# Performance work log

Hardware: AMD Instinct MI355X
Metric: run time of the kernel (lower is better)

Reference implementation:

```python
import jax, jax.numpy as jnp
import numpy as np

N = 50000
E = 800000
IN_DIM = 256
HID = 64
HEADS = 4
OUT_DIM = 32
NEG_SLOPE = 0.2


def gat_conv(x, edge_index, W, a_src, a_dst, bias, heads, out_ch, concat):
    """PyG-style GATConv (eval mode, add_self_loops=True).
    x: [N, F_in]; edge_index: [2, E'] with row0=src, row1=dst.
    W: [F_in, heads*out_ch]; a_src/a_dst: [heads, out_ch]; bias: [heads*out_ch] or [out_ch].
    """
    n = x.shape[0]
    # add self loops
    loops = jnp.arange(n, dtype=edge_index.dtype)
    src = jnp.concatenate([edge_index[0], loops])
    dst = jnp.concatenate([edge_index[1], loops])

    h = (x @ W).reshape(n, heads, out_ch)              # [N, H, C]
    alpha_s = jnp.einsum('nhc,hc->nh', h, a_src)       # [N, H]
    alpha_d = jnp.einsum('nhc,hc->nh', h, a_dst)       # [N, H]
    e = alpha_s[src] + alpha_d[dst]                    # [E', H]
    e = jnp.where(e >= 0, e, NEG_SLOPE * e)            # leaky_relu

    # segment softmax over incoming edges of each dst node
    m = jax.ops.segment_max(e, dst, num_segments=n)    # [N, H]
    ex = jnp.exp(e - m[dst])
    denom = jax.ops.segment_sum(ex, dst, num_segments=n)
    alpha = ex / (denom[dst] + 1e-16)                  # [E', H]

    msg = h[src] * alpha[:, :, None]                   # [E', H, C]
    out = jax.ops.segment_sum(msg, dst, num_segments=n)  # [N, H, C]
    out = out.reshape(n, heads * out_ch) if concat else out.mean(axis=1)
    return out + bias


def setup_inputs() -> dict:
    key = jax.random.key(0)
    ks = jax.random.split(key, 10)
    x = jax.random.normal(ks[0], (N, IN_DIM), dtype=jnp.float32)
    edge_index = jax.random.randint(ks[1], (2, E), 0, N, dtype=jnp.int32)
    s1 = 1.0 / np.sqrt(IN_DIM)
    s2 = 1.0 / np.sqrt(HEADS * HID)
    return {
        'x': x,
        'edge_index': edge_index,
        'W1': jax.random.normal(ks[2], (IN_DIM, HEADS * HID), dtype=jnp.float32) * s1,
        'a_src1': jax.random.normal(ks[3], (HEADS, HID), dtype=jnp.float32) * s2,
        'a_dst1': jax.random.normal(ks[4], (HEADS, HID), dtype=jnp.float32) * s2,
        'b1': jnp.zeros((HEADS * HID,), dtype=jnp.float32),
        'W2': jax.random.normal(ks[5], (HEADS * HID, OUT_DIM), dtype=jnp.float32) * s2,
        'a_src2': jax.random.normal(ks[6], (1, OUT_DIM), dtype=jnp.float32) * 0.125,
        'a_dst2': jax.random.normal(ks[7], (1, OUT_DIM), dtype=jnp.float32) * 0.125,
        'b2': jnp.zeros((OUT_DIM,), dtype=jnp.float32),
    }


def reference(x, edge_index, W1, a_src1, a_dst1, b1, W2, a_src2, a_dst2, b2):
    h = gat_conv(x, edge_index, W1, a_src1, a_dst1, b1, HEADS, HID, concat=True)
    h = jax.nn.elu(h)
    out = gat_conv(h, edge_index, W2, a_src2, a_dst2, b2, 1, OUT_DIM, concat=False)
    return out
```

## Files before the change

kernel.cpp:

```cpp
#include <hip/hip_runtime.h>

#define NEG_SLOPE 0.2f
#define CAP 64
#define LOG2E 1.44269504f

typedef short bf16x8 __attribute__((ext_vector_type(8)));
typedef float f32x4 __attribute__((ext_vector_type(4)));
typedef _Float16 half4v __attribute__((ext_vector_type(4)));
typedef _Float16 half8v __attribute__((ext_vector_type(8)));

__device__ inline short bf16_rne(float x) {
    unsigned u = __float_as_uint(x);
    unsigned r = u + 0x7FFFu + ((u >> 16) & 1u);
    return (short)(r >> 16);
}

__device__ inline float fast_exp2(float x) {
#if __has_builtin(__builtin_amdgcn_exp2f)
    return __builtin_amdgcn_exp2f(x);
#else
    return exp2f(x);
#endif
}


__global__ void k_prepw(const float* __restrict__ W1, short* __restrict__ Wt,
                        const float* __restrict__ W2, _Float16* __restrict__ W2t,
                        int* __restrict__ cursor, int* __restrict__ col, int N) {
    int r = blockIdx.x;
    int t = threadIdx.x;
    Wt[(size_t)t * 256 + r] = bf16_rne(W1[(size_t)r * 256 + t]);
    if (t < 32) W2t[(size_t)t * 256 + r] = (_Float16)W2[(size_t)r * 32 + t];
    int gid = blockIdx.x * 256 + threadIdx.x;
    if (gid < N) {
        cursor[gid] = 1;
        col[(size_t)gid * CAP] = gid;
    }
}


__global__ __launch_bounds__(256) void k_gemm1_scatter(
        const float* __restrict__ x, const short* __restrict__ Wt,
        const float* __restrict__ a_src, const float* __restrict__ a_dst,
        _Float16* __restrict__ h1, float* __restrict__ as1, float* __restrict__ ad1, int N,
        const int* __restrict__ srcI, const int* __restrict__ dstI,
        int* __restrict__ cursor, int* __restrict__ col, int E) {
    __shared__ short Ab[64 * 40];
    __shared__ short Bb[256 * 40];
    const int tid = threadIdx.x;
    const int b = blockIdx.x;
    const int nGemm = gridDim.x;

    const int chunk = (E + nGemm - 1) / nGemm;
    const int ss = b * chunk;
    const int se = (ss + chunk < E) ? (ss + chunk) : E;
    const int jb = ss + tid * 4;
    int4 d4 = make_int4(0, 0, 0, 0), s4 = make_int4(0, 0, 0, 0);
    int p0 = CAP, p1 = CAP, p2 = CAP, p3 = CAP;
    const bool quad = (jb + 3 < se);
    if (quad) {
        d4 = *(const int4*)(dstI + jb);
        s4 = *(const int4*)(srcI + jb);
    } else if (jb < se) {
        for (int i = jb; i < se; ++i) {
            int d = dstI[i];
            int p = atomicAdd(&cursor[d], 1);
            if (p < CAP) col[(size_t)d * CAP + p] = srcI[i];
        }
    }

    const int lane = tid & 63;
    const int wc = tid >> 6;
    const int row0 = b * 64;
    const int m15 = lane & 15, quad4 = lane >> 4;

    f32x4 acc[4][4] = {};

    const int arow = tid >> 2;
    const int akseg = (tid & 3) * 8;

#pragma unroll
    for (int kk = 0; kk < 8; ++kk) {
        const int k0 = kk * 32;
        {
            int row = row0 + arow;
            float vals[8];
            if (row < N) {
                float4 v0 = *(const float4*)(x + (size_t)row * 256 + k0 + akseg);
                float4 v1 = *(const float4*)(x + (size_t)row * 256 + k0 + akseg + 4);
                vals[0] = v0.x; vals[1] = v0.y; vals[2] = v0.z; vals[3] = v0.w;
                vals[4] = v1.x; vals[5] = v1.y; vals[6] = v1.z; vals[7] = v1.w;
            } else {
#pragma unroll
                for (int i = 0; i < 8; ++i) vals[i] = 0.f;
            }
            short buf[8];
#pragma unroll
            for (int i = 0; i < 8; ++i) buf[i] = bf16_rne(vals[i]);
            *(bf16x8*)&Ab[arow * 40 + akseg] = *(bf16x8*)&buf[0];
        }
        {
#pragma unroll
            for (int s = 0; s < 4; ++s)
                *(bf16x8*)&Bb[tid * 40 + s * 8] =
                    *(const bf16x8*)(Wt + (size_t)tid * 256 + k0 + s * 8);
        }
        if (quad) {
            const int e = kk >> 1;
            const int d = (e == 0) ? d4.x : (e == 1) ? d4.y : (e == 2) ? d4.z : d4.w;
            if ((kk & 1) == 0) {
                int pr = atomicAdd(&cursor[d], 1);
                if (e == 0) p0 = pr; else if (e == 1) p1 = pr;
                else if (e == 2) p2 = pr; else p3 = pr;
            } else {
                const int s = (e == 0) ? s4.x : (e == 1) ? s4.y : (e == 2) ? s4.z : s4.w;
                const int pr = (e == 0) ? p0 : (e == 1) ? p1 : (e == 2) ? p2 : p3;
                if (pr < CAP) col[(size_t)d * CAP + pr] = s;
            }
        }
        __syncthreads();
        bf16x8 ab[4];
#pragma unroll
        for (int mt = 0; mt < 4; ++mt)
            ab[mt] = *(const bf16x8*)&Ab[(mt * 16 + m15) * 40 + quad4 * 8];
#pragma unroll
        for (int nt = 0; nt < 4; ++nt) {
            int nn = wc * 64 + nt * 16 + m15;
            bf16x8 bb = *(const bf16x8*)&Bb[nn * 40 + quad4 * 8];
#pragma unroll
            for (int mt = 0; mt < 4; ++mt)
                acc[mt][nt] = __builtin_amdgcn_mfma_f32_16x16x32_bf16(ab[mt], bb, acc[mt][nt], 0, 0, 0);
        }
        __syncthreads();
    }
    const int head = wc;
#pragma unroll
    for (int mt = 0; mt < 4; ++mt) {
        float va[4] = {0.f, 0.f, 0.f, 0.f};
        float vd[4] = {0.f, 0.f, 0.f, 0.f};
#pragma unroll
        for (int nt = 0; nt < 4; ++nt) {
            int colg = wc * 64 + nt * 16 + m15;
            float asv = a_src[colg];
            float adv = a_dst[colg];
#pragma unroll
            for (int r = 0; r < 4; ++r) {
                float accv = acc[mt][nt][r];
                int row = row0 + mt * 16 + quad4 * 4 + r;
                if (row < N) h1[(size_t)row * 256 + colg] = (_Float16)accv;
                va[r] = fmaf(accv, asv, va[r]);
                vd[r] = fmaf(accv, adv, vd[r]);
            }
        }
#pragma unroll
        for (int r = 0; r < 4; ++r) {
#pragma unroll
            for (int mq = 1; mq < 16; mq <<= 1) {
                va[r] += __shfl_xor(va[r], mq);
                vd[r] += __shfl_xor(vd[r], mq);
            }
            int row = row0 + mt * 16 + quad4 * 4 + r;
            if (m15 == 0 && row < N) {
                as1[(size_t)row * 4 + head] = va[r] * LOG2E;
                ad1[(size_t)row * 4 + head] = vd[r] * LOG2E;
            }
        }
    }
}


__global__ __launch_bounds__(256) void k_fuse1(
        const _Float16* __restrict__ h1, const float* __restrict__ as1,
        const float* __restrict__ ad1, const int* __restrict__ cursor,
        const int* __restrict__ col, const float* __restrict__ b1,
        const _Float16* __restrict__ W2t, const float* __restrict__ a_s2,
        const float* __restrict__ a_d2, _Float16* __restrict__ z,
        float* __restrict__ as2, float* __restrict__ ad2, int N) {
    __shared__ _Float16 W2s[32 * 264];
    __shared__ _Float16 h2s[4 * 256];
    const int tid = threadIdx.x;
    const int l = tid & 63;
    const int wave = tid >> 6;
    const int n = blockIdx.x * 4 + wave;

    for (int i8 = tid; i8 < 1024; i8 += 256) {
        int elem = i8 * 8;
        int row = elem >> 8, k = elem & 255;
        *(half8v*)&W2s[row * 264 + k] = *(const half8v*)(W2t + (size_t)row * 256 + k);
    }
    __syncthreads();
    if (n >= N) return;

    const int head = l >> 4;
    const int beg = n * CAP;
    int deg = __builtin_amdgcn_readfirstlane(cursor[n]);
    if (deg > CAP) deg = CAP;
    int colv = 0;
    if (l < deg) colv = col[beg + l];
    float adv = ad1[(size_t)n * 4 + head];

    f32x4 a0 = {}, a1 = {}, a2 = {}, a3 = {};
    float s0 = 0.f, s1 = 0.f, s2 = 0.f, s3 = 0.f;
    int j = 0;
    for (; j + 3 < deg; j += 4) {
        int c0 = __builtin_amdgcn_readlane(colv, j);
        int c1 = __builtin_amdgcn_readlane(colv, j + 1);
        int c2 = __builtin_amdgcn_readlane(colv, j + 2);
        int c3 = __builtin_amdgcn_readlane(colv, j + 3);
        float e0 = as1[(size_t)c0 * 4 + head] + adv;
        float e1 = as1[(size_t)c1 * 4 + head] + adv;
        float e2 = as1[(size_t)c2 * 4 + head] + adv;
        float e3 = as1[(size_t)c3 * 4 + head] + adv;
        e0 = fmaxf(e0, NEG_SLOPE * e0); e1 = fmaxf(e1, NEG_SLOPE * e1);
        e2 = fmaxf(e2, NEG_SLOPE * e2); e3 = fmaxf(e3, NEG_SLOPE * e3);
        float p0 = fast_exp2(e0), p1 = fast_exp2(e1);
        float p2 = fast_exp2(e2), p3 = fast_exp2(e3);
        half4v h0 = *((const half4v*)(h1 + (size_t)c0 * 256) + l);
        half4v hv1 = *((const half4v*)(h1 + (size_t)c1 * 256) + l);
        half4v h2 = *((const half4v*)(h1 + (size_t)c2 * 256) + l);
        half4v h3 = *((const half4v*)(h1 + (size_t)c3 * 256) + l);
        s0 += p0; s1 += p1; s2 += p2; s3 += p3;
        a0 += __builtin_convertvector(h0, f32x4) * p0;
        a1 += __builtin_convertvector(hv1, f32x4) * p1;
        a2 += __builtin_convertvector(h2, f32x4) * p2;
        a3 += __builtin_convertvector(h3, f32x4) * p3;
    }
    for (; j < deg; ++j) {
        int c0 = __builtin_amdgcn_readlane(colv, j);
        float e0 = as1[(size_t)c0 * 4 + head] + adv;
        e0 = fmaxf(e0, NEG_SLOPE * e0);
        float p0 = fast_exp2(e0);
        half4v h0 = *((const half4v*)(h1 + (size_t)c0 * 256) + l);
        s0 += p0;
        a0 += __builtin_convertvector(h0, f32x4) * p0;
    }
    f32x4 at = (a0 + a1) + (a2 + a3);
    float iv = 1.f / ((s0 + s1) + (s2 + s3) + 1e-16f);
    float4 bb = *(const float4*)(b1 + l * 4);
    float4 v;
    v.x = at[0] * iv + bb.x;
    v.y = at[1] * iv + bb.y;
    v.z = at[2] * iv + bb.z;
    v.w = at[3] * iv + bb.w;
    v.x = (v.x > 0.f) ? v.x : (__expf(v.x) - 1.f);
    v.y = (v.y > 0.f) ? v.y : (__expf(v.y) - 1.f);
    v.z = (v.z > 0.f) ? v.z : (__expf(v.z) - 1.f);
    v.w = (v.w > 0.f) ? v.w : (__expf(v.w) - 1.f);
    half4v hv;
    hv.x = (_Float16)v.x; hv.y = (_Float16)v.y; hv.z = (_Float16)v.z; hv.w = (_Float16)v.w;
    *((half4v*)(h2s + wave * 256) + l) = hv;

    int c = l & 31;
    int kh = (l >> 5) * 128;
    const _Float16* hrow = h2s + wave * 256 + kh;
    const _Float16* wrow = W2s + c * 264 + kh;
    float accz = 0.f;
#pragma unroll
    for (int k = 0; k < 128; k += 8) {
        half8v hz = *(const half8v*)(hrow + k);
        half8v wz = *(const half8v*)(wrow + k);
#if __has_builtin(__builtin_amdgcn_fdot2)
        accz = __builtin_amdgcn_fdot2(__builtin_shufflevector(hz, hz, 0, 1),
                                      __builtin_shufflevector(wz, wz, 0, 1), accz, false);
        accz = __builtin_amdgcn_fdot2(__builtin_shufflevector(hz, hz, 2, 3),
                                      __builtin_shufflevector(wz, wz, 2, 3), accz, false);
        accz = __builtin_amdgcn_fdot2(__builtin_shufflevector(hz, hz, 4, 5),
                                      __builtin_shufflevector(wz, wz, 4, 5), accz, false);
        accz = __builtin_amdgcn_fdot2(__builtin_shufflevector(hz, hz, 6, 7),
                                      __builtin_shufflevector(wz, wz, 6, 7), accz, false);
#else
        accz = fmaf((float)hz[0], (float)wz[0], accz);
        accz = fmaf((float)hz[1], (float)wz[1], accz);
        accz = fmaf((float)hz[2], (float)wz[2], accz);
        accz = fmaf((float)hz[3], (float)wz[3], accz);
        accz = fmaf((float)hz[4], (float)wz[4], accz);
        accz = fmaf((float)hz[5], (float)wz[5], accz);
        accz = fmaf((float)hz[6], (float)wz[6], accz);
        accz = fmaf((float)hz[7], (float)wz[7], accz);
#endif
    }
    accz += __shfl_xor(accz, 32);
    float za = accz * a_s2[c];
    float zd = accz * a_d2[c];
#pragma unroll
    for (int mq = 1; mq < 32; mq <<= 1) {
        za += __shfl_xor(za, mq);
        zd += __shfl_xor(zd, mq);
    }
    if (l < 32) z[(size_t)n * 32 + c] = (_Float16)accz;
    if (l == 0) {
        as2[n] = za * LOG2E;
        ad2[n] = zd * LOG2E;
    }
}


__global__ void k_gather2(const _Float16* __restrict__ z, const float* __restrict__ as2,
                          const float* __restrict__ ad2, const int* __restrict__ cursor,
                          const int* __restrict__ col, const float* __restrict__ b2,
                          float* __restrict__ out, int N) {
    int n = blockIdx.x * 4 + (threadIdx.x >> 6);
    if (n >= N) return;
    int l = threadIdx.x & 63;
    int eo = l >> 3;
    int cg = l & 7;
    int beg = n * CAP;
    int deg = __builtin_amdgcn_readfirstlane(cursor[n]);
    if (deg > CAP) deg = CAP;
    int colv = 0;
    if (l < deg) colv = col[beg + l];
    float adn = ad2[n];

    const int nst = (deg + 7) >> 3;

    float av_[8];
    half4v zv_[8];
#pragma unroll
    for (int t = 0; t < 8; ++t) {
        if (t < nst) {
            int idx = t * 8 + eo;
            int sidx = (idx < deg) ? idx : 0;
            int src = __shfl(colv, sidx);
            av_[t] = as2[src];
            zv_[t] = *((const half4v*)(z + (size_t)src * 32) + cg);
        }
    }

    f32x4 acc = {};
    float s = 0.f;
#pragma unroll
    for (int t = 0; t < 8; ++t) {
        if (t < nst) {
            int idx = t * 8 + eo;
            float e = av_[t] + adn;
            e = fmaxf(e, NEG_SLOPE * e);
            float p = (idx < deg) ? fast_exp2(e) : 0.f;
            s += p;
            acc += __builtin_convertvector(zv_[t], f32x4) * p;
        }
    }

    float ax = acc[0], ay = acc[1], az = acc[2], aw = acc[3];
#pragma unroll
    for (int mq = 8; mq < 64; mq <<= 1) {
        ax += __shfl_xor(ax, mq);
        ay += __shfl_xor(ay, mq);
        az += __shfl_xor(az, mq);
        aw += __shfl_xor(aw, mq);
        s += __shfl_xor(s, mq);
    }
    if (eo == 0) {
        float iv = 1.f / (s + 1e-16f);
        float4 bb = *(const float4*)(b2 + cg * 4);
        float4 v;
        v.x = ax * iv + bb.x;
        v.y = ay * iv + bb.y;
        v.z = az * iv + bb.z;
        v.w = aw * iv + bb.w;
        *(float4*)(out + (size_t)n * 32 + cg * 4) = v;
    }
}


extern "C" void kernel_launch(void* const* d_in, const int* in_sizes, int n_in,
                              void* d_out, int out_size, void* d_ws, size_t ws_size,
                              hipStream_t stream) {
    const float* x    = (const float*)d_in[0];
    const int*   ei   = (const int*)d_in[1];
    const float* W1   = (const float*)d_in[2];
    const float* a_s1 = (const float*)d_in[3];
    const float* a_d1 = (const float*)d_in[4];
    const float* b1   = (const float*)d_in[5];
    const float* W2   = (const float*)d_in[6];
    const float* a_s2 = (const float*)d_in[7];
    const float* a_d2 = (const float*)d_in[8];
    const float* b2   = (const float*)d_in[9];
    float* out = (float*)d_out;

    const int N = in_sizes[0] / 256;
    const int E = in_sizes[1] / 2;
    const int* srcIdx = ei;
    const int* dstIdx = ei + E;

    char* ws = (char*)d_ws;
    size_t off = 0;
    auto alloc = [&](size_t bytes) {
        void* p = ws + off;
        off += (bytes + 255) & ~(size_t)255;
        return p;
    };
    _Float16* h1   = (_Float16*)alloc((size_t)N * 256 * 2);
    _Float16* z    = (_Float16*)alloc((size_t)N * 32 * 2);
    float* as1    = (float*)alloc((size_t)N * 16);
    float* ad1    = (float*)alloc((size_t)N * 16);
    float* as2    = (float*)alloc((size_t)N * 4);
    float* ad2    = (float*)alloc((size_t)N * 4);
    short* Wt     = (short*)alloc((size_t)256 * 256 * 2);
    _Float16* W2t = (_Float16*)alloc((size_t)32 * 256 * 2);
    int*   cursor = (int*)alloc((size_t)N * 4);
    int*   col    = (int*)alloc((size_t)N * CAP * 4);

    k_prepw<<<256, 256, 0, stream>>>(W1, Wt, W2, W2t, cursor, col, N);

    const int nGemm = (N + 63) / 64;
    k_gemm1_scatter<<<nGemm, 256, 0, stream>>>(x, Wt, a_s1, a_d1, h1, as1, ad1, N,
                                               srcIdx, dstIdx, cursor, col, E);

    k_fuse1<<<(N + 3) / 4, 256, 0, stream>>>(h1, as1, ad1, cursor, col, b1, W2t,
                                             a_s2, a_d2, z, as2, ad2, N);

    k_gather2<<<(N + 3) / 4, 256, 0, stream>>>(z, as2, ad2, cursor, col, b2, out, N);
}
```

Measured before the change: 245.2 us.

## Recompute source attention scores from gathered features instead of storing them

The per-node source attention logits (as1, as2) are no longer computed and stored in the producer kernels. Each gather kernel instead recomputes them from the already-gathered neighbor feature rows, using a dot product with a_src and a cross-lane shuffle reduction. This removes a dependent scattered load per edge and the stores of as1/as2, in exchange for extra shuffles and FMAs per edge. It also changes numerics slightly, because the scores are now computed from fp16-rounded features.

New measurement: 258.8 us. 5.5% more time.

```diff
diff --git a/kernel.cpp b/kernel.cpp
--- a/kernel.cpp
+++ b/kernel.cpp
@@ -41,8 +41,8 @@
 
 __global__ __launch_bounds__(256) void k_gemm1_scatter(
         const float* __restrict__ x, const short* __restrict__ Wt,
-        const float* __restrict__ a_src, const float* __restrict__ a_dst,
-        _Float16* __restrict__ h1, float* __restrict__ as1, float* __restrict__ ad1, int N,
+        const float* __restrict__ a_dst,
+        _Float16* __restrict__ h1, float* __restrict__ ad1, int N,
         const int* __restrict__ srcI, const int* __restrict__ dstI,
         int* __restrict__ cursor, int* __restrict__ col, int E) {
     __shared__ short Ab[64 * 40];
@@ -136,46 +136,39 @@
     const int head = wc;
 #pragma unroll
     for (int mt = 0; mt < 4; ++mt) {
-        float va[4] = {0.f, 0.f, 0.f, 0.f};
         float vd[4] = {0.f, 0.f, 0.f, 0.f};
 #pragma unroll
         for (int nt = 0; nt < 4; ++nt) {
             int colg = wc * 64 + nt * 16 + m15;
-            float asv = a_src[colg];
             float adv = a_dst[colg];
 #pragma unroll
             for (int r = 0; r < 4; ++r) {
                 float accv = acc[mt][nt][r];
                 int row = row0 + mt * 16 + quad4 * 4 + r;
                 if (row < N) h1[(size_t)row * 256 + colg] = (_Float16)accv;
-                va[r] = fmaf(accv, asv, va[r]);
                 vd[r] = fmaf(accv, adv, vd[r]);
             }
         }
 #pragma unroll
         for (int r = 0; r < 4; ++r) {
 #pragma unroll
-            for (int mq = 1; mq < 16; mq <<= 1) {
-                va[r] += __shfl_xor(va[r], mq);
+            for (int mq = 1; mq < 16; mq <<= 1)
                 vd[r] += __shfl_xor(vd[r], mq);
-            }
             int row = row0 + mt * 16 + quad4 * 4 + r;
-            if (m15 == 0 && row < N) {
-                as1[(size_t)row * 4 + head] = va[r] * LOG2E;
+            if (m15 == 0 && row < N)
                 ad1[(size_t)row * 4 + head] = vd[r] * LOG2E;
-            }
         }
     }
 }
 
 
 __global__ __launch_bounds__(256) void k_fuse1(
-        const _Float16* __restrict__ h1, const float* __restrict__ as1,
+        const _Float16* __restrict__ h1, const float* __restrict__ a_s1,
         const float* __restrict__ ad1, const int* __restrict__ cursor,
         const int* __restrict__ col, const float* __restrict__ b1,
-        const _Float16* __restrict__ W2t, const float* __restrict__ a_s2,
+        const _Float16* __restrict__ W2t,
         const float* __restrict__ a_d2, _Float16* __restrict__ z,
-        float* __restrict__ as2, float* __restrict__ ad2, int N) {
+        float* __restrict__ ad2, int N) {
     __shared__ _Float16 W2s[32 * 264];
     __shared__ _Float16 h2s[4 * 256];
     const int tid = threadIdx.x;
@@ -198,8 +191,20 @@
     int colv = 0;
     if (l < deg) colv = col[beg + l];
     float adv = ad1[(size_t)n * 4 + head];
-
-    f32x4 a0 = {}, a1 = {}, a2 = {}, a3 = {};
+    const float4 a1v = *(const float4*)(a_s1 + 4 * l);
+
+#define EDOT(HV, OUT)                                                            \
+    {                                                                            \
+        float t_ = fmaf((float)HV.x, a1v.x, fmaf((float)HV.y, a1v.y,             \
+                   fmaf((float)HV.z, a1v.z, (float)HV.w * a1v.w)));              \
+        t_ += __shfl_xor(t_, 1);                                                 \
+        t_ += __shfl_xor(t_, 2);                                                 \
+        t_ += __shfl_xor(t_, 4);                                                 \
+        t_ += __shfl_xor(t_, 8);                                                 \
+        OUT = t_;                                                                \
+    }
+
+    f32x4 a0 = {}, a1a = {}, a2 = {}, a3 = {};
     float s0 = 0.f, s1 = 0.f, s2 = 0.f, s3 = 0.f;
     int j = 0;
     for (; j + 3 < deg; j += 4) {
@@ -207,34 +212,37 @@
         int c1 = __builtin_amdgcn_readlane(colv, j + 1);
         int c2 = __builtin_amdgcn_readlane(colv, j + 2);
         int c3 = __builtin_amdgcn_readlane(colv, j + 3);
-        float e0 = as1[(size_t)c0 * 4 + head] + adv;
-        float e1 = as1[(size_t)c1 * 4 + head] + adv;
-        float e2 = as1[(size_t)c2 * 4 + head] + adv;
-        float e3 = as1[(size_t)c3 * 4 + head] + adv;
+        half4v h0 = *((const half4v*)(h1 + (size_t)c0 * 256) + l);
+        half4v hv1 = *((const half4v*)(h1 + (size_t)c1 * 256) + l);
+        half4v h2 = *((const half4v*)(h1 + (size_t)c2 * 256) + l);
+        half4v h3 = *((const half4v*)(h1 + (size_t)c3 * 256) + l);
+        float d0, d1, d2, d3;
+        EDOT(h0, d0) EDOT(hv1, d1) EDOT(h2, d2) EDOT(h3, d3)
+        float e0 = fmaf(d0, LOG2E, adv), e1 = fmaf(d1, LOG2E, adv);
+        float e2 = fmaf(d2, LOG2E, adv), e3 = fmaf(d3, LOG2E, adv);
         e0 = fmaxf(e0, NEG_SLOPE * e0); e1 = fmaxf(e1, NEG_SLOPE * e1);
         e2 = fmaxf(e2, NEG_SLOPE * e2); e3 = fmaxf(e3, NEG_SLOPE * e3);
         float p0 = fast_exp2(e0), p1 = fast_exp2(e1);
         float p2 = fast_exp2(e2), p3 = fast_exp2(e3);
-        half4v h0 = *((const half4v*)(h1 + (size_t)c0 * 256) + l);
-        half4v hv1 = *((const half4v*)(h1 + (size_t)c1 * 256) + l);
-        half4v h2 = *((const half4v*)(h1 + (size_t)c2 * 256) + l);
-        half4v h3 = *((const half4v*)(h1 + (size_t)c3 * 256) + l);
         s0 += p0; s1 += p1; s2 += p2; s3 += p3;
         a0 += __builtin_convertvector(h0, f32x4) * p0;
-        a1 += __builtin_convertvector(hv1, f32x4) * p1;
+        a1a += __builtin_convertvector(hv1, f32x4) * p1;
         a2 += __builtin_convertvector(h2, f32x4) * p2;
         a3 += __builtin_convertvector(h3, f32x4) * p3;
     }
     for (; j < deg; ++j) {
         int c0 = __builtin_amdgcn_readlane(colv, j);
-        float e0 = as1[(size_t)c0 * 4 + head] + adv;
+        half4v h0 = *((const half4v*)(h1 + (size_t)c0 * 256) + l);
+        float d0;
+        EDOT(h0, d0)
+        float e0 = fmaf(d0, LOG2E, adv);
         e0 = fmaxf(e0, NEG_SLOPE * e0);
         float p0 = fast_exp2(e0);
-        half4v h0 = *((const half4v*)(h1 + (size_t)c0 * 256) + l);
         s0 += p0;
         a0 += __builtin_convertvector(h0, f32x4) * p0;
     }
-    f32x4 at = (a0 + a1) + (a2 + a3);
+#undef EDOT
+    f32x4 at = (a0 + a1a) + (a2 + a3);
     float iv = 1.f / ((s0 + s1) + (s2 + s3) + 1e-16f);
     float4 bb = *(const float4*)(b1 + l * 4);
     float4 v;
@@ -280,22 +288,16 @@
 #endif
     }
     accz += __shfl_xor(accz, 32);
-    float za = accz * a_s2[c];
     float zd = accz * a_d2[c];
 #pragma unroll
-    for (int mq = 1; mq < 32; mq <<= 1) {
-        za += __shfl_xor(za, mq);
+    for (int mq = 1; mq < 32; mq <<= 1)
         zd += __shfl_xor(zd, mq);
-    }
     if (l < 32) z[(size_t)n * 32 + c] = (_Float16)accz;
-    if (l == 0) {
-        as2[n] = za * LOG2E;
-        ad2[n] = zd * LOG2E;
-    }
-}
-
-
-__global__ void k_gather2(const _Float16* __restrict__ z, const float* __restrict__ as2,
+    if (l == 0) ad2[n] = zd * LOG2E;
+}
+
+
+__global__ void k_gather2(const _Float16* __restrict__ z, const float* __restrict__ a_s2,
                           const float* __restrict__ ad2, const int* __restrict__ cursor,
                           const int* __restrict__ col, const float* __restrict__ b2,
                           float* __restrict__ out, int N) {
@@ -310,10 +312,10 @@
     int colv = 0;
     if (l < deg) colv = col[beg + l];
     float adn = ad2[n];
+    const float4 a2v = *(const float4*)(a_s2 + 4 * cg);
 
     const int nst = (deg + 7) >> 3;
 
-    float av_[8];
     half4v zv_[8];
 #pragma unroll
     for (int t = 0; t < 8; ++t) {
@@ -321,7 +323,6 @@
             int idx = t * 8 + eo;
             int sidx = (idx < deg) ? idx : 0;
             int src = __shfl(colv, sidx);
-            av_[t] = as2[src];
             zv_[t] = *((const half4v*)(z + (size_t)src * 32) + cg);
         }
     }
@@ -332,7 +333,12 @@
     for (int t = 0; t < 8; ++t) {
         if (t < nst) {
             int idx = t * 8 + eo;
-            float e = av_[t] + adn;
+            float d_ = fmaf((float)zv_[t].x, a2v.x, fmaf((float)zv_[t].y, a2v.y,
+                       fmaf((float)zv_[t].z, a2v.z, (float)zv_[t].w * a2v.w)));
+            d_ += __shfl_xor(d_, 1);
+            d_ += __shfl_xor(d_, 2);
+            d_ += __shfl_xor(d_, 4);
+            float e = fmaf(d_, LOG2E, adn);
             e = fmaxf(e, NEG_SLOPE * e);
             float p = (idx < deg) ? fast_exp2(e) : 0.f;
             s += p;
@@ -391,9 +397,7 @@
     };
     _Float16* h1   = (_Float16*)alloc((size_t)N * 256 * 2);
     _Float16* z    = (_Float16*)alloc((size_t)N * 32 * 2);
-    float* as1    = (float*)alloc((size_t)N * 16);
     float* ad1    = (float*)alloc((size_t)N * 16);
-    float* as2    = (float*)alloc((size_t)N * 4);
     float* ad2    = (float*)alloc((size_t)N * 4);
     short* Wt     = (short*)alloc((size_t)256 * 256 * 2);
     _Float16* W2t = (_Float16*)alloc((size_t)32 * 256 * 2);
@@ -403,11 +407,11 @@
     k_prepw<<<256, 256, 0, stream>>>(W1, Wt, W2, W2t, cursor, col, N);
 
     const int nGemm = (N + 63) / 64;
-    k_gemm1_scatter<<<nGemm, 256, 0, stream>>>(x, Wt, a_s1, a_d1, h1, as1, ad1, N,
+    k_gemm1_scatter<<<nGemm, 256, 0, stream>>>(x, Wt, a_d1, h1, ad1, N,
                                                srcIdx, dstIdx, cursor, col, E);
 
-    k_fuse1<<<(N + 3) / 4, 256, 0, stream>>>(h1, as1, ad1, cursor, col, b1, W2t,
-                                             a_s2, a_d2, z, as2, ad2, N);
-
-    k_gather2<<<(N + 3) / 4, 256, 0, stream>>>(z, as2, ad2, cursor, col, b2, out, N);
-}
+    k_fuse1<<<(N + 3) / 4, 256, 0, stream>>>(h1, a_s1, ad1, cursor, col, b1, W2t,
+                                             a_d2, z, ad2, N);
+
+    k_gather2<<<(N + 3) / 4, 256, 0, stream>>>(z, a_s2, ad2, cursor, col, b2, out, N);
+}
```
